# Kernel tuning notes

Measured on AMD Instinct MI355X. Metric: run time of the kernel, lower is better.

## Reference

```python
import jax, jax.numpy as jnp
import numpy as np

DIM = 1024
HEADS = 16
SCALE = DIM ** -0.5  # note: source scales by full dim, not head dim


def setup_inputs() -> dict:
    key = jax.random.key(0)
    k1, k2, k3 = jax.random.split(key, 3)
    b, n = 2, 2048
    x = jax.random.normal(k1, (b, n, DIM), dtype=jnp.float32)
    w_qkv = jax.random.normal(k2, (3 * DIM, DIM), dtype=jnp.float32) * (DIM ** -0.5)
    w_out = jax.random.normal(k3, (DIM, DIM), dtype=jnp.float32) * (DIM ** -0.5)
    b_out = jnp.zeros((DIM,), dtype=jnp.float32)
    return {"x": x, "w_qkv": w_qkv, "w_out": w_out, "b_out": b_out}


def reference(x, w_qkv, w_out, b_out):
    b, n, d = x.shape
    h = HEADS
    hd = d // h
    # torch Linear: y = x @ W.T
    qkv = x @ w_qkv.T  # [b, n, 3d]
    q, k, v = jnp.split(qkv, 3, axis=-1)
    # reshape to [b, h, n, hd]
    def to_heads(t):
        return t.reshape(b, n, h, hd).transpose(0, 2, 1, 3)
    q, k, v = to_heads(q), to_heads(k), to_heads(v)
    dots = jnp.einsum('bhqd,bhkd->bhqk', q, k) * SCALE
    attn = jax.nn.softmax(dots, axis=-1)
    out = jnp.einsum('bhqk,bhkd->bhqd', attn, v)
    out = out.transpose(0, 2, 1, 3).reshape(b, n, d)
    return out @ w_out.T + b_out
```

## Files before the change

kernel.cpp:

```cpp
#include <hip/hip_runtime.h>

typedef __attribute__((ext_vector_type(8))) _Float16 half8;
typedef __attribute__((ext_vector_type(4))) _Float16 half4;
typedef __attribute__((ext_vector_type(2))) __fp16 fp16x2;
typedef __attribute__((ext_vector_type(4))) float f32x4;
typedef __attribute__((ext_vector_type(4))) unsigned int u32x4;
typedef __attribute__((ext_vector_type(2))) unsigned int u32x2;

#define NSEQ 2048
#define DIMM 1024
#define NH   16
#define HD   64

typedef const void __attribute__((address_space(1))) gvoid_t;
typedef void __attribute__((address_space(3))) svoid_t;

__device__ __forceinline__ void gload_lds16(const void* g, void* l) {
  __builtin_amdgcn_global_load_lds((gvoid_t*)g, (svoid_t*)l, 16, 0, 0);
}

union H2U { fp16x2 h; unsigned int u; };

__global__ __launch_bounds__(256) void cvt_all(const float* __restrict__ x,
                                               const float* __restrict__ wqkv,
                                               const float* __restrict__ wout,
                                               _Float16* __restrict__ xh,
                                               _Float16* __restrict__ wqkvh,
                                               _Float16* __restrict__ wouth) {
  int i = blockIdx.x * 256 + threadIdx.x;
  const float* src;
  _Float16* dst;
  int off;
  if (i < 524288) { src = x; dst = xh; off = i; }
  else if (i < 917504) { src = wqkv; dst = wqkvh; off = i - 524288; }
  else { src = wout; dst = wouth; off = i - 917504; }
  const float4* p = (const float4*)src + (size_t)off * 2;
  float4 v0 = p[0], v1 = p[1];
  half8 h;
  h[0] = (_Float16)v0.x; h[1] = (_Float16)v0.y; h[2] = (_Float16)v0.z; h[3] = (_Float16)v0.w;
  h[4] = (_Float16)v1.x; h[5] = (_Float16)v1.y; h[6] = (_Float16)v1.z; h[7] = (_Float16)v1.w;
  *((half8*)dst + off) = h;
}

__device__ __forceinline__ void gemm_mainloop(const _Float16* __restrict__ A,
                                              const _Float16* __restrict__ B,
                                              int am0, int bn0,
                                              _Float16* As, _Float16* Bs,
                                              f32x4 acc[4][4]) {
  const int tid = threadIdx.x;
  const int w = tid >> 6, lane = tid & 63;
  const int lr = lane >> 2;
  const int lc = (lane & 3) * 8;
  const int wm = (w >> 1) * 64, wn = (w & 1) * 64;
  const int g = lane >> 4, ln = lane & 15;

  for (int k0 = 0; k0 < 1024; k0 += 32) {
#pragma unroll
    for (int rr = 0; rr < 4; ++rr) {
      int c = rr * 4 + w;
      if (c < 8) {
        gload_lds16(A + (size_t)(am0 + c * 16 + lr) * 1024 + k0 + lc, As + c * 512);
      } else {
        int cb = c - 8;
        gload_lds16(B + (size_t)(bn0 + cb * 16 + lr) * 1024 + k0 + lc, Bs + cb * 512);
      }
    }
    __syncthreads();
    half8 af[4], bf[4];
#pragma unroll
    for (int mi = 0; mi < 4; ++mi)
      af[mi] = *(const half8*)(As + (wm + mi * 16 + ln) * 32 + g * 8);
#pragma unroll
    for (int ni = 0; ni < 4; ++ni)
      bf[ni] = *(const half8*)(Bs + (wn + ni * 16 + ln) * 32 + g * 8);
#pragma unroll
    for (int mi = 0; mi < 4; ++mi)
#pragma unroll
      for (int ni = 0; ni < 4; ++ni)
        acc[mi][ni] = __builtin_amdgcn_mfma_f32_16x16x32_f16(af[mi], bf[ni], acc[mi][ni], 0, 0, 0);
    __syncthreads();
  }
}

union SmemQKV {
  struct { _Float16 a[128 * 32]; _Float16 b[128 * 32]; } ab;
  _Float16 t[128 * 136];
};

#define QSCALE 0.0450843450f

__global__ __launch_bounds__(256) void gemm_qkv(const _Float16* __restrict__ x,
                                                const _Float16* __restrict__ wqkv,
                                                _Float16* __restrict__ qh,
                                                _Float16* __restrict__ kh,
                                                _Float16* __restrict__ vt) {
  __shared__ SmemQKV sh;
  f32x4 acc[4][4];
#pragma unroll
  for (int i = 0; i < 4; ++i)
#pragma unroll
    for (int j = 0; j < 4; ++j) acc[i][j] = (f32x4){0.f, 0.f, 0.f, 0.f};
  const int bm = blockIdx.x, bn = blockIdx.y;
  gemm_mainloop(x, wqkv, bm * 128, bn * 128, sh.ab.a, sh.ab.b, acc);

  const int tid = threadIdx.x;
  const int w = tid >> 6, lane = tid & 63;
  const int g = lane >> 4, ln = lane & 15;
  const int wm = (w >> 1) * 64, wn = (w & 1) * 64;
  const int sec = bn >> 3;
  const int cbase = (bn & 7) * 128;

  if (sec < 2) {
    _Float16* dst = (sec == 0) ? qh : kh;
    const float scale = (sec == 0) ? QSCALE : 1.0f;
#pragma unroll
    for (int mi = 0; mi < 4; ++mi) {
      int row = bm * 128 + wm + mi * 16 + g * 4;
      int bidx = row >> 11, nidx = row & 2047;
#pragma unroll
      for (int ni = 0; ni < 4; ++ni) {
        int col = cbase + wn + ni * 16 + ln;
        int h = col >> 6, d = col & 63;
        _Float16* p = dst + ((size_t)(bidx * NH + h) * NSEQ + nidx) * HD + d;
#pragma unroll
        for (int r = 0; r < 4; ++r) p[r * HD] = (_Float16)(acc[mi][ni][r] * scale);
      }
    }
  } else {
    __syncthreads();
#pragma unroll
    for (int mi = 0; mi < 4; ++mi)
#pragma unroll
      for (int ni = 0; ni < 4; ++ni)
#pragma unroll
        for (int r = 0; r < 4; ++r)
          sh.t[(wn + ni * 16 + ln) * 136 + wm + mi * 16 + g * 4 + r] = (_Float16)acc[mi][ni][r];
    __syncthreads();
    const int row0 = bm * 128;
    const int bidx = row0 >> 11, n0 = row0 & 2047;
#pragma unroll
    for (int i = 0; i < 8; ++i) {
      int ci = i * 256 + tid;
      int drow = ci >> 4, nofs = (ci & 15) * 8;
      int col = cbase + drow;
      int h = col >> 6, d = col & 63;
      u32x4 val = *(const u32x4*)(sh.t + drow * 136 + nofs);
      *(u32x4*)(vt + ((size_t)(bidx * NH + h) * HD + d) * NSEQ + n0 + nofs) = val;
    }
  }
}

__global__ __launch_bounds__(256, 2) void attn_fwd(const _Float16* __restrict__ qg,
                                                   const _Float16* __restrict__ kg,
                                                   const _Float16* __restrict__ vg,
                                                   _Float16* __restrict__ ao) {
  __shared__ _Float16 Ks[3][64 * 64];
  __shared__ _Float16 Vs[3][64 * 64];
  __shared__ _Float16 Ps[4][32 * 64];

  const int bid = blockIdx.x;
  const int swz = (bid & 7) * 64 + (bid >> 3);
  const int bh = swz >> 4, qt = swz & 15;
  const int tid = threadIdx.x, w = tid >> 6, lane = tid & 63;
  const int g = lane >> 4, ln = lane & 15;
  const int sw8 = ln & 7;

  const _Float16* qp = qg + (size_t)bh * NSEQ * HD;
  const _Float16* kp = kg + (size_t)bh * NSEQ * HD;
  const _Float16* vp = vg + (size_t)bh * HD * NSEQ;
  char* psw = (char*)&Ps[w][0];

  const int qr = qt * 128 + w * 32;

  half8 qf[2][2];
#pragma unroll
  for (int qb = 0; qb < 2; ++qb)
#pragma unroll
    for (int dk = 0; dk < 2; ++dk)
      qf[qb][dk] = *(const half8*)(qp + (size_t)(qr + qb * 16 + ln) * HD + dk * 32 + g * 8);
  asm volatile("" ::: "memory");

  const int rsub = lane >> 3;
  const int csw = ((lane & 7) ^ rsub) << 3;
  const int c0 = 2 * w;

#define STAGE(buf, tt)                                                              \
  {                                                                                 \
    const _Float16* kt_ = kp + (size_t)(tt) * 64 * HD;                              \
    _Pragma("unroll")                                                               \
    for (int i = 0; i < 2; ++i) {                                                   \
      int c = c0 + i;                                                               \
      gload_lds16(kt_ + (size_t)(c * 8 + rsub) * HD + csw, &Ks[buf][c * 512]);      \
    }                                                                               \
    _Pragma("unroll")                                                               \
    for (int i = 0; i < 2; ++i) {                                                   \
      int c = c0 + i;                                                               \
      gload_lds16(vp + (size_t)(c * 8 + rsub) * NSEQ + (tt) * 64 + csw,             \
                  &Vs[buf][c * 512]);                                               \
    }                                                                               \
  }

  STAGE(0, 0);
  STAGE(1, 1);

  float lsum[2] = {0.f, 0.f};
  f32x4 oacc[4][2];
#pragma unroll
  for (int sd = 0; sd < 4; ++sd)
#pragma unroll
    for (int qb = 0; qb < 2; ++qb) oacc[sd][qb] = (f32x4){0.f, 0.f, 0.f, 0.f};
  const f32x4 fz = (f32x4){0.f, 0.f, 0.f, 0.f};

#define TILE_BODY(kbuf, vbuf)                                                       \
  {                                                                                 \
    const _Float16* kb_ = (kbuf);                                                   \
    const _Float16* vb_ = (vbuf);                                                   \
    f32x4 sacc[4][2];                                                               \
    __builtin_amdgcn_s_setprio(1);                                                  \
    _Pragma("unroll")                                                               \
    for (int s = 0; s < 4; ++s) {                                                   \
      const _Float16* kr = kb_ + (s * 16 + ln) * 64;                                \
      half8 kf0 = *(const half8*)(kr + ((g ^ sw8) << 3));                           \
      half8 kf1 = *(const half8*)(kr + (((4 + g) ^ sw8) << 3));                     \
      sacc[s][0] = __builtin_amdgcn_mfma_f32_16x16x32_f16(kf0, qf[0][0], fz, 0, 0, 0);            \
      sacc[s][0] = __builtin_amdgcn_mfma_f32_16x16x32_f16(kf1, qf[0][1], sacc[s][0], 0, 0, 0);    \
      sacc[s][1] = __builtin_amdgcn_mfma_f32_16x16x32_f16(kf0, qf[1][0], fz, 0, 0, 0);            \
      sacc[s][1] = __builtin_amdgcn_mfma_f32_16x16x32_f16(kf1, qf[1][1], sacc[s][1], 0, 0, 0);    \
    }                                                                               \
    __builtin_amdgcn_s_setprio(0);                                                  \
    half8 vf[4][2];           \
    _Pragma("unroll")                                                               \
    for (int sd = 0; sd < 4; ++sd) {                                                \
      const _Float16* vr = vb_ + (sd * 16 + ln) * 64;                               \
      vf[sd][0] = *(const half8*)(vr + ((g ^ sw8) << 3));                           \
      vf[sd][1] = *(const half8*)(vr + (((4 + g) ^ sw8) << 3));                     \
    }                                                                               \
    _Pragma("unroll")                                                               \
    for (int qb = 0; qb < 2; ++qb) {                                                \
      const int q = qb * 16 + ln;                                                   \
      float rs = 0.f;                                                               \
      _Pragma("unroll")                                                             \
      for (int s = 0; s < 4; ++s) {                                                 \
        float e0 = __builtin_amdgcn_exp2f(sacc[s][qb][0]);                          \
        float e1 = __builtin_amdgcn_exp2f(sacc[s][qb][1]);                          \
        float e2 = __builtin_amdgcn_exp2f(sacc[s][qb][2]);                          \
        float e3 = __builtin_amdgcn_exp2f(sacc[s][qb][3]);                          \
        rs += (e0 + e1) + (e2 + e3);                                                \
        H2U a_, b_;                                                                 \
        a_.h = __builtin_amdgcn_cvt_pkrtz(e0, e1);                                  \
        b_.h = __builtin_amdgcn_cvt_pkrtz(e2, e3);                                  \
        u32x2 quad; quad[0] = a_.u; quad[1] = b_.u;                                 \
        const int kq = s * 4 + g;                                                   \
        *(u32x2*)(psw + q * 128 + ((kq ^ ln) << 3)) = quad;                         \
      }                                                                             \
      lsum[qb] += rs;                                                               \
    }                                                                               \
    asm volatile("s_waitcnt lgkmcnt(0)" ::: "memory");  \
    half8 pb[2][2];                                                                 \
    _Pragma("unroll")                                                               \
    for (int qb = 0; qb < 2; ++qb) {                                                \
      const int q = qb * 16 + ln;                                                   \
      _Pragma("unroll")                                                             \
      for (int f = 0; f < 2; ++f) {                                                 \
        const int qd = (f * 4 + g) * 2;                                             \
        u32x2 lo = *(const u32x2*)(psw + q * 128 + ((qd ^ ln) << 3));               \
        u32x2 hi = *(const u32x2*)(psw + q * 128 + (((qd + 1) ^ ln) << 3));         \
        union { u32x4 u; half8 h; } pk;                                             \
        pk.u[0] = lo[0]; pk.u[1] = lo[1]; pk.u[2] = hi[0]; pk.u[3] = hi[1];         \
        pb[qb][f] = pk.h;                                                           \
      }                                                                             \
    }                                                                               \
    __builtin_amdgcn_s_setprio(1);                                                  \
    _Pragma("unroll")                                                               \
    for (int sd = 0; sd < 4; ++sd) {                                                \
      _Pragma("unroll")                                                             \
      for (int qb = 0; qb < 2; ++qb) {                                              \
        oacc[sd][qb] = __builtin_amdgcn_mfma_f32_16x16x32_f16(vf[sd][0], pb[qb][0], oacc[sd][qb], 0, 0, 0); \
        oacc[sd][qb] = __builtin_amdgcn_mfma_f32_16x16x32_f16(vf[sd][1], pb[qb][1], oacc[sd][qb], 0, 0, 0); \
      }                                                                             \
    }                                                                               \
    __builtin_amdgcn_s_setprio(0);                                                  \
  }

  for (int t = 0; t < 30; ++t) {
    asm volatile("s_waitcnt vmcnt(4)" ::: "memory");
    __builtin_amdgcn_s_barrier();
    STAGE((t + 2) % 3, t + 2);
    TILE_BODY(&Ks[t % 3][0], &Vs[t % 3][0])
  }
  {
    asm volatile("s_waitcnt vmcnt(4)" ::: "memory");
    __builtin_amdgcn_s_barrier();
    TILE_BODY(&Ks[0][0], &Vs[0][0])
  }
  {
    asm volatile("s_waitcnt vmcnt(0)" ::: "memory");
    __builtin_amdgcn_s_barrier();
    TILE_BODY(&Ks[1][0], &Vs[1][0])
  }

  const int bidx = bh >> 4, h = bh & 15;
#pragma unroll
  for (int qb = 0; qb < 2; ++qb) {
    lsum[qb] += __shfl_xor(lsum[qb], 16, 64);
    lsum[qb] += __shfl_xor(lsum[qb], 32, 64);
    const float inv = 1.f / lsum[qb];
    const int n = qr + qb * 16 + ln;
#pragma unroll
    for (int sd = 0; sd < 4; ++sd) {
      half4 o4;
#pragma unroll
      for (int r = 0; r < 4; ++r) o4[r] = (_Float16)(oacc[sd][qb][r] * inv);
      *(half4*)(ao + (size_t)(bidx * NSEQ + n) * DIMM + h * HD + sd * 16 + g * 4) = o4;
    }
  }
}

__global__ __launch_bounds__(256) void gemm_out(const _Float16* __restrict__ ao,
                                                const _Float16* __restrict__ wout,
                                                const float* __restrict__ bias,
                                                float* __restrict__ out) {
  __shared__ _Float16 As[128 * 32];
  __shared__ _Float16 Bs[128 * 32];
  f32x4 acc[4][4];
#pragma unroll
  for (int i = 0; i < 4; ++i)
#pragma unroll
    for (int j = 0; j < 4; ++j) acc[i][j] = (f32x4){0.f, 0.f, 0.f, 0.f};
  const int bm = blockIdx.x, bn = blockIdx.y;
  gemm_mainloop(ao, wout, bm * 128, bn * 128, As, Bs, acc);
  const int tid = threadIdx.x;
  const int w = tid >> 6, lane = tid & 63;
  const int g = lane >> 4, ln = lane & 15;
  const int wm = (w >> 1) * 64, wn = (w & 1) * 64;
#pragma unroll
  for (int mi = 0; mi < 4; ++mi) {
    const int row = bm * 128 + wm + mi * 16 + g * 4;
#pragma unroll
    for (int ni = 0; ni < 4; ++ni) {
      const int col = bn * 128 + wn + ni * 16 + ln;
      const float b = bias[col];
#pragma unroll
      for (int r = 0; r < 4; ++r) out[(size_t)(row + r) * DIMM + col] = acc[mi][ni][r] + b;
    }
  }
}

extern "C" void kernel_launch(void* const* d_in, const int* in_sizes, int n_in,
                              void* d_out, int out_size, void* d_ws, size_t ws_size,
                              hipStream_t stream) {
  const float* x    = (const float*)d_in[0];
  const float* wqkv = (const float*)d_in[1];
  const float* wout = (const float*)d_in[2];
  const float* bout = (const float*)d_in[3];
  float* out = (float*)d_out;

  _Float16* ws = (_Float16*)d_ws;
  _Float16* x_h    = ws;
  _Float16* wqkv_h = ws + (4u << 20);
  _Float16* wout_h = ws + (7u << 20);
  _Float16* q_h    = ws + (8u << 20);
  _Float16* k_h    = ws + (12u << 20);
  _Float16* vt_h   = ws + (16u << 20);
  _Float16* ao_h   = ws + (20u << 20);

  cvt_all<<<dim3(4096), 256, 0, stream>>>(x, wqkv, wout, x_h, wqkv_h, wout_h);
  gemm_qkv<<<dim3(32, 24), 256, 0, stream>>>(x_h, wqkv_h, q_h, k_h, vt_h);
  attn_fwd<<<dim3(512), 256, 0, stream>>>(q_h, k_h, vt_h, ao_h);
  gemm_out<<<dim3(32, 8), 256, 0, stream>>>(ao_h, wout_h, bout, out);
}
```

Measured before the change: 115.4 us.

## Software-pipeline QK^T of next tile with softmax and PV of current tile

Restructures the attention inner loop so the QK^T MFMAs for tile t+1 are issued between the two softmax halves of tile t, using double-buffered score accumulators (saccA/saccB) and rotating buffer indices. This is meant to overlap exp/convert VALU work with matrix-core work and hide LDS latency. Each iteration now waits with vmcnt(0) instead of vmcnt(4), which shrinks the prefetch depth and may expose global-load latency. The extra live accumulators also raise register pressure, which could hurt occupancy.

```diff
diff --git a/kernel.cpp b/kernel.cpp
--- a/kernel.cpp
+++ b/kernel.cpp
@@ -211,51 +211,46 @@
     for (int qb = 0; qb < 2; ++qb) oacc[sd][qb] = (f32x4){0.f, 0.f, 0.f, 0.f};
   const f32x4 fz = (f32x4){0.f, 0.f, 0.f, 0.f};
 
-#define TILE_BODY(kbuf, vbuf)                                                       \
-  {                                                                                 \
-    const _Float16* kb_ = (kbuf);                                                   \
-    const _Float16* vb_ = (vbuf);                                                   \
-    f32x4 sacc[4][2];                                                               \
-    __builtin_amdgcn_s_setprio(1);                                                  \
+#define QK_PHASE(SN, nb)                                                            \
+  {                                                                                 \
+    const _Float16* kb_ = &Ks[0][0] + (nb) * 4096;                                  \
+    half8 kf0, kf1;                                                                 \
     _Pragma("unroll")                                                               \
     for (int s = 0; s < 4; ++s) {                                                   \
       const _Float16* kr = kb_ + (s * 16 + ln) * 64;                                \
-      half8 kf0 = *(const half8*)(kr + ((g ^ sw8) << 3));                           \
-      half8 kf1 = *(const half8*)(kr + (((4 + g) ^ sw8) << 3));                     \
-      sacc[s][0] = __builtin_amdgcn_mfma_f32_16x16x32_f16(kf0, qf[0][0], fz, 0, 0, 0);            \
-      sacc[s][0] = __builtin_amdgcn_mfma_f32_16x16x32_f16(kf1, qf[0][1], sacc[s][0], 0, 0, 0);    \
-      sacc[s][1] = __builtin_amdgcn_mfma_f32_16x16x32_f16(kf0, qf[1][0], fz, 0, 0, 0);            \
-      sacc[s][1] = __builtin_amdgcn_mfma_f32_16x16x32_f16(kf1, qf[1][1], sacc[s][1], 0, 0, 0);    \
-    }                                                                               \
-    __builtin_amdgcn_s_setprio(0);                                                  \
-    half8 vf[4][2];           \
-    _Pragma("unroll")                                                               \
-    for (int sd = 0; sd < 4; ++sd) {                                                \
-      const _Float16* vr = vb_ + (sd * 16 + ln) * 64;                               \
-      vf[sd][0] = *(const half8*)(vr + ((g ^ sw8) << 3));                           \
-      vf[sd][1] = *(const half8*)(vr + (((4 + g) ^ sw8) << 3));                     \
-    }                                                                               \
-    _Pragma("unroll")                                                               \
-    for (int qb = 0; qb < 2; ++qb) {                                                \
-      const int q = qb * 16 + ln;                                                   \
-      float rs = 0.f;                                                               \
-      _Pragma("unroll")                                                             \
-      for (int s = 0; s < 4; ++s) {                                                 \
-        float e0 = __builtin_amdgcn_exp2f(sacc[s][qb][0]);                          \
-        float e1 = __builtin_amdgcn_exp2f(sacc[s][qb][1]);                          \
-        float e2 = __builtin_amdgcn_exp2f(sacc[s][qb][2]);                          \
-        float e3 = __builtin_amdgcn_exp2f(sacc[s][qb][3]);                          \
-        rs += (e0 + e1) + (e2 + e3);                                                \
-        H2U a_, b_;                                                                 \
-        a_.h = __builtin_amdgcn_cvt_pkrtz(e0, e1);                                  \
-        b_.h = __builtin_amdgcn_cvt_pkrtz(e2, e3);                                  \
-        u32x2 quad; quad[0] = a_.u; quad[1] = b_.u;                                 \
-        const int kq = s * 4 + g;                                                   \
-        *(u32x2*)(psw + q * 128 + ((kq ^ ln) << 3)) = quad;                         \
-      }                                                                             \
-      lsum[qb] += rs;                                                               \
-    }                                                                               \
-    asm volatile("s_waitcnt lgkmcnt(0)" ::: "memory");  \
+      kf0 = *(const half8*)(kr + ((g ^ sw8) << 3));                                 \
+      kf1 = *(const half8*)(kr + (((4 + g) ^ sw8) << 3));                           \
+      SN[s][0] = __builtin_amdgcn_mfma_f32_16x16x32_f16(kf0, qf[0][0], fz, 0, 0, 0);        \
+      SN[s][0] = __builtin_amdgcn_mfma_f32_16x16x32_f16(kf1, qf[0][1], SN[s][0], 0, 0, 0);  \
+      SN[s][1] = __builtin_amdgcn_mfma_f32_16x16x32_f16(kf0, qf[1][0], fz, 0, 0, 0);        \
+      SN[s][1] = __builtin_amdgcn_mfma_f32_16x16x32_f16(kf1, qf[1][1], SN[s][1], 0, 0, 0);  \
+    }                                                                               \
+  }
+
+#define SM_HALF(SC, qb)                                                             \
+  {                                                                                 \
+    const int q = (qb) * 16 + ln;                                                   \
+    float rs = 0.f;                                                                 \
+    _Pragma("unroll")                                                               \
+    for (int s = 0; s < 4; ++s) {                                                   \
+      float e0 = __builtin_amdgcn_exp2f(SC[s][qb][0]);                              \
+      float e1 = __builtin_amdgcn_exp2f(SC[s][qb][1]);                              \
+      float e2 = __builtin_amdgcn_exp2f(SC[s][qb][2]);                              \
+      float e3 = __builtin_amdgcn_exp2f(SC[s][qb][3]);                              \
+      rs += (e0 + e1) + (e2 + e3);                                                  \
+      H2U a_, b_;                                                                   \
+      a_.h = __builtin_amdgcn_cvt_pkrtz(e0, e1);                                    \
+      b_.h = __builtin_amdgcn_cvt_pkrtz(e2, e3);                                    \
+      u32x2 quad; quad[0] = a_.u; quad[1] = b_.u;                                   \
+      const int kq = s * 4 + g;                                                     \
+      *(u32x2*)(psw + q * 128 + ((kq ^ ln) << 3)) = quad;                           \
+    }                                                                               \
+    lsum[qb] += rs;                                                                 \
+  }
+
+#define PV_PHASE(vf_)                                                               \
+  {                                                                                 \
+    asm volatile("s_waitcnt lgkmcnt(0)" ::: "memory");                              \
     half8 pb[2][2];                                                                 \
     _Pragma("unroll")                                                               \
     for (int qb = 0; qb < 2; ++qb) {                                                \
@@ -275,28 +270,55 @@
     for (int sd = 0; sd < 4; ++sd) {                                                \
       _Pragma("unroll")                                                             \
       for (int qb = 0; qb < 2; ++qb) {                                              \
-        oacc[sd][qb] = __builtin_amdgcn_mfma_f32_16x16x32_f16(vf[sd][0], pb[qb][0], oacc[sd][qb], 0, 0, 0); \
-        oacc[sd][qb] = __builtin_amdgcn_mfma_f32_16x16x32_f16(vf[sd][1], pb[qb][1], oacc[sd][qb], 0, 0, 0); \
+        oacc[sd][qb] = __builtin_amdgcn_mfma_f32_16x16x32_f16(vf_[sd][0], pb[qb][0], oacc[sd][qb], 0, 0, 0); \
+        oacc[sd][qb] = __builtin_amdgcn_mfma_f32_16x16x32_f16(vf_[sd][1], pb[qb][1], oacc[sd][qb], 0, 0, 0); \
       }                                                                             \
     }                                                                               \
     __builtin_amdgcn_s_setprio(0);                                                  \
   }
 
-  for (int t = 0; t < 30; ++t) {
-    asm volatile("s_waitcnt vmcnt(4)" ::: "memory");
-    __builtin_amdgcn_s_barrier();
-    STAGE((t + 2) % 3, t + 2);
-    TILE_BODY(&Ks[t % 3][0], &Vs[t % 3][0])
-  }
+#define VF_READ(vf_, cb)                                                            \
+  {                                                                                 \
+    const _Float16* vb_ = &Vs[0][0] + (cb) * 4096;                                  \
+    _Pragma("unroll")                                                               \
+    for (int sd = 0; sd < 4; ++sd) {                                                \
+      const _Float16* vr = vb_ + (sd * 16 + ln) * 64;                               \
+      vf_[sd][0] = *(const half8*)(vr + ((g ^ sw8) << 3));                          \
+      vf_[sd][1] = *(const half8*)(vr + (((4 + g) ^ sw8) << 3));                    \
+    }                                                                               \
+  }
+
+#define BODY(SC, SN, tt, DO_STAGE)                                                  \
+  {                                                                                 \
+    asm volatile("s_waitcnt vmcnt(0)" ::: "memory");         \
+    __builtin_amdgcn_s_barrier();                         \
+    if (DO_STAGE) STAGE(stg, (tt) + 2);                                             \
+    SM_HALF(SC, 0)                                                                  \
+    QK_PHASE(SN, nxt)                        \
+    half8 vf_[4][2];                                                                \
+    VF_READ(vf_, cur)                                                               \
+    SM_HALF(SC, 1)                                                                  \
+    PV_PHASE(vf_)                                                                   \
+    int tmp_ = cur; cur = nxt; nxt = stg; stg = tmp_;                               \
+  }
+
+  asm volatile("s_waitcnt vmcnt(4)" ::: "memory");
+  __builtin_amdgcn_s_barrier();
+  f32x4 saccA[4][2], saccB[4][2];
+  int cur = 0, nxt = 1, stg = 2;
+  QK_PHASE(saccA, 0)
+
+  for (int t = 0; t < 30; t += 2) {
+    BODY(saccA, saccB, t, 1)
+    BODY(saccB, saccA, t + 1, 1)
+  }
+  BODY(saccA, saccB, 30, 0)
   {
-    asm volatile("s_waitcnt vmcnt(4)" ::: "memory");
-    __builtin_amdgcn_s_barrier();
-    TILE_BODY(&Ks[0][0], &Vs[0][0])
-  }
-  {
-    asm volatile("s_waitcnt vmcnt(0)" ::: "memory");
-    __builtin_amdgcn_s_barrier();
-    TILE_BODY(&Ks[1][0], &Vs[1][0])
+    half8 vf_[4][2];
+    VF_READ(vf_, cur)
+    SM_HALF(saccB, 0)
+    SM_HALF(saccB, 1)
+    PV_PHASE(vf_)
   }
 
   const int bidx = bh >> 4, h = bh & 15;
```

New measurement: 116.6 us. Within noise of the previous version (+1.1%).

## Permute K rows at load so softmax probabilities feed PV MFMA directly from registers

Applied to the files above, without the earlier changes.

K rows are loaded into LDS in a permuted order so that the S accumulator layout produced by the QK^T MFMA matches the B-operand layout needed for the PV MFMA. The per-warp LDS scratch for P, its write, the lgkmcnt wait and the readback are removed, and exponentials are packed straight into half8 registers. This cuts LDS traffic and a synchronization point in the inner loop. The risk is correctness: the column permutation of K must match V's key order exactly, and it only works because the key index mapping is consistent within the tile.

```diff
diff --git a/kernel.cpp b/kernel.cpp
--- a/kernel.cpp
+++ b/kernel.cpp
@@ -156,7 +156,6 @@
                                                    _Float16* __restrict__ ao) {
   __shared__ _Float16 Ks[3][64 * 64];
   __shared__ _Float16 Vs[3][64 * 64];
-  __shared__ _Float16 Ps[4][32 * 64];
 
   const int bid = blockIdx.x;
   const int swz = (bid & 7) * 64 + (bid >> 3);
@@ -168,7 +167,6 @@
   const _Float16* qp = qg + (size_t)bh * NSEQ * HD;
   const _Float16* kp = kg + (size_t)bh * NSEQ * HD;
   const _Float16* vp = vg + (size_t)bh * HD * NSEQ;
-  char* psw = (char*)&Ps[w][0];
 
   const int qr = qt * 128 + w * 32;
 
@@ -183,21 +181,19 @@
   const int rsub = lane >> 3;
   const int csw = ((lane & 7) ^ rsub) << 3;
   const int c0 = 2 * w;
+  const int R0 = c0 * 8 + rsub, R1 = R0 + 8;
+  const int ks0 = 32 * (R0 >> 5) + 8 * ((R0 >> 2) & 3) + 4 * ((R0 >> 4) & 1) + (R0 & 3);
+  const int ks1 = 32 * (R1 >> 5) + 8 * ((R1 >> 2) & 3) + 4 * ((R1 >> 4) & 1) + (R1 & 3);
 
 #define STAGE(buf, tt)                                                              \
   {                                                                                 \
     const _Float16* kt_ = kp + (size_t)(tt) * 64 * HD;                              \
-    _Pragma("unroll")                                                               \
-    for (int i = 0; i < 2; ++i) {                                                   \
-      int c = c0 + i;                                                               \
-      gload_lds16(kt_ + (size_t)(c * 8 + rsub) * HD + csw, &Ks[buf][c * 512]);      \
-    }                                                                               \
-    _Pragma("unroll")                                                               \
-    for (int i = 0; i < 2; ++i) {                                                   \
-      int c = c0 + i;                                                               \
-      gload_lds16(vp + (size_t)(c * 8 + rsub) * NSEQ + (tt) * 64 + csw,             \
-                  &Vs[buf][c * 512]);                                               \
-    }                                                                               \
+    gload_lds16(kt_ + (size_t)ks0 * HD + csw, &Ks[buf][c0 * 512]);                  \
+    gload_lds16(kt_ + (size_t)ks1 * HD + csw, &Ks[buf][(c0 + 1) * 512]);            \
+    gload_lds16(vp + (size_t)(c0 * 8 + rsub) * NSEQ + (tt) * 64 + csw,              \
+                &Vs[buf][c0 * 512]);                                                \
+    gload_lds16(vp + (size_t)((c0 + 1) * 8 + rsub) * NSEQ + (tt) * 64 + csw,        \
+                &Vs[buf][(c0 + 1) * 512]);                                          \
   }
 
   STAGE(0, 0);
@@ -228,47 +224,41 @@
       sacc[s][1] = __builtin_amdgcn_mfma_f32_16x16x32_f16(kf1, qf[1][1], sacc[s][1], 0, 0, 0);    \
     }                                                                               \
     __builtin_amdgcn_s_setprio(0);                                                  \
-    half8 vf[4][2];           \
+    half8 vf[4][2];                                                                 \
     _Pragma("unroll")                                                               \
     for (int sd = 0; sd < 4; ++sd) {                                                \
       const _Float16* vr = vb_ + (sd * 16 + ln) * 64;                               \
       vf[sd][0] = *(const half8*)(vr + ((g ^ sw8) << 3));                           \
       vf[sd][1] = *(const half8*)(vr + (((4 + g) ^ sw8) << 3));                     \
     }                                                                               \
+    half8 pb[2][2];                                                                 \
     _Pragma("unroll")                                                               \
     for (int qb = 0; qb < 2; ++qb) {                                                \
-      const int q = qb * 16 + ln;                                                   \
+      float e[4][4];                                                                \
       float rs = 0.f;                                                               \
       _Pragma("unroll")                                                             \
       for (int s = 0; s < 4; ++s) {                                                 \
-        float e0 = __builtin_amdgcn_exp2f(sacc[s][qb][0]);                          \
-        float e1 = __builtin_amdgcn_exp2f(sacc[s][qb][1]);                          \
-        float e2 = __builtin_amdgcn_exp2f(sacc[s][qb][2]);                          \
-        float e3 = __builtin_amdgcn_exp2f(sacc[s][qb][3]);                          \
-        rs += (e0 + e1) + (e2 + e3);                                                \
-        H2U a_, b_;                                                                 \
-        a_.h = __builtin_amdgcn_cvt_pkrtz(e0, e1);                                  \
-        b_.h = __builtin_amdgcn_cvt_pkrtz(e2, e3);                                  \
-        u32x2 quad; quad[0] = a_.u; quad[1] = b_.u;                                 \
-        const int kq = s * 4 + g;                                                   \
-        *(u32x2*)(psw + q * 128 + ((kq ^ ln) << 3)) = quad;                         \
+        e[s][0] = __builtin_amdgcn_exp2f(sacc[s][qb][0]);                           \
+        e[s][1] = __builtin_amdgcn_exp2f(sacc[s][qb][1]);                           \
+        e[s][2] = __builtin_amdgcn_exp2f(sacc[s][qb][2]);                           \
+        e[s][3] = __builtin_amdgcn_exp2f(sacc[s][qb][3]);                           \
+        rs += (e[s][0] + e[s][1]) + (e[s][2] + e[s][3]);                            \
       }                                                                             \
       lsum[qb] += rs;                                                               \
-    }                                                                               \
-    asm volatile("s_waitcnt lgkmcnt(0)" ::: "memory");  \
-    half8 pb[2][2];                                                                 \
-    _Pragma("unroll")                                                               \
-    for (int qb = 0; qb < 2; ++qb) {                                                \
-      const int q = qb * 16 + ln;                                                   \
-      _Pragma("unroll")                                                             \
-      for (int f = 0; f < 2; ++f) {                                                 \
-        const int qd = (f * 4 + g) * 2;                                             \
-        u32x2 lo = *(const u32x2*)(psw + q * 128 + ((qd ^ ln) << 3));               \
-        u32x2 hi = *(const u32x2*)(psw + q * 128 + (((qd + 1) ^ ln) << 3));         \
-        union { u32x4 u; half8 h; } pk;                                             \
-        pk.u[0] = lo[0]; pk.u[1] = lo[1]; pk.u[2] = hi[0]; pk.u[3] = hi[1];         \
-        pb[qb][f] = pk.h;                                                           \
-      }                                                                             \
+      H2U c00, c01, c10, c11, c20, c21, c30, c31;                                   \
+      c00.h = __builtin_amdgcn_cvt_pkrtz(e[0][0], e[0][1]);                         \
+      c01.h = __builtin_amdgcn_cvt_pkrtz(e[0][2], e[0][3]);                         \
+      c10.h = __builtin_amdgcn_cvt_pkrtz(e[1][0], e[1][1]);                         \
+      c11.h = __builtin_amdgcn_cvt_pkrtz(e[1][2], e[1][3]);                         \
+      c20.h = __builtin_amdgcn_cvt_pkrtz(e[2][0], e[2][1]);                         \
+      c21.h = __builtin_amdgcn_cvt_pkrtz(e[2][2], e[2][3]);                         \
+      c30.h = __builtin_amdgcn_cvt_pkrtz(e[3][0], e[3][1]);                         \
+      c31.h = __builtin_amdgcn_cvt_pkrtz(e[3][2], e[3][3]);                         \
+      union { u32x4 u; half8 h; } p0, p1;                                           \
+      p0.u[0] = c00.u; p0.u[1] = c01.u; p0.u[2] = c10.u; p0.u[3] = c11.u;           \
+      p1.u[0] = c20.u; p1.u[1] = c21.u; p1.u[2] = c30.u; p1.u[3] = c31.u;           \
+      pb[qb][0] = p0.h;                                                             \
+      pb[qb][1] = p1.h;                                                             \
     }                                                                               \
     __builtin_amdgcn_s_setprio(1);                                                  \
     _Pragma("unroll")                                                               \
```

Result: faster. 107.7 us (-6.7%).
